# Kernel optimization log

Hardware: AMD Instinct MI355X
Metric: run time of the kernel (lower is better)

Reference implementation:

```python
import jax, jax.numpy as jnp
import numpy as np

E = 8        # n_experts
H = 1024     # hidden_size == input_size
M = 2048     # intermediate_size
K = 2        # topk
SE = 1       # share_expert
BSZ, SEQ = 2, 1024
W_SCALE = 0.02


def setup_inputs() -> dict:
    key = jax.random.key(0)
    ks = jax.random.split(key, 9)
    return {
        "x": jax.random.normal(ks[0], (BSZ, SEQ, H), jnp.float32),
        "gate_w": jax.random.normal(ks[1], (E, H), jnp.float32) * W_SCALE,
        "beta": jnp.zeros((E,), jnp.float32),
        "gate_proj_w": jax.random.normal(ks[2], (E, H, M), jnp.float32) * W_SCALE,
        "up_proj_w": jax.random.normal(ks[3], (E, H, M), jnp.float32) * W_SCALE,
        "down_proj_w": jax.random.normal(ks[4], (E, M, H), jnp.float32) * W_SCALE,
        "shared_gate_w": jax.random.normal(ks[5], (SE, H, M), jnp.float32) * W_SCALE,
        "shared_up_w": jax.random.normal(ks[6], (SE, H, M), jnp.float32) * W_SCALE,
        "shared_down_w": jax.random.normal(ks[7], (SE, M, H), jnp.float32) * W_SCALE,
    }


def reference(x, gate_w, beta, gate_proj_w, up_proj_w, down_proj_w,
              shared_gate_w, shared_up_w, shared_down_w):
    B0, S0, H0 = x.shape
    xt = x.reshape(-1, H0)                       # [B, H], B = B0*S0 tokens
    B = xt.shape[0]

    # --- routing: top-k on (logits + beta), gate prob = sigmoid(selected logits) ---
    logits = xt @ gate_w.T                       # [B, E]
    _, idx = jax.lax.top_k(logits + beta, K)     # [B, K] expert indices
    probs = jax.nn.sigmoid(jnp.take_along_axis(logits, idx, axis=-1))  # [B, K]

    # combine weights c[b, e]: scatter top-k probs (equivalent to index_add combine)
    c = jnp.zeros((B, E), xt.dtype).at[jnp.arange(B)[:, None], idx].add(probs)

    # --- per-expert SwiGLU over all tokens, then weighted combine by c ---
    g = jnp.einsum('bh,ehm->bem', xt, gate_proj_w)   # [B, E, M]
    u = jnp.einsum('bh,ehm->bem', xt, up_proj_w)     # [B, E, M]
    h = jax.nn.silu(g) * u                           # [B, E, M]
    eo = jnp.einsum('bem,emh->beh', h, down_proj_w)  # [B, E, H]
    combined = jnp.einsum('beh,be->bh', eo, c)       # [B, H]

    # --- shared expert(s): applied to every token, no gating ---
    sg = jnp.einsum('bh,ehm->bem', xt, shared_gate_w)
    su = jnp.einsum('bh,ehm->bem', xt, shared_up_w)
    sh = jax.nn.silu(sg) * su
    shared_out = jnp.einsum('bem,emh->beh', sh, shared_down_w).sum(axis=1)  # [B, H]

    return (combined + shared_out).reshape(B0, S0, H0)
```

## Files before the change

### kernel.cpp

```cpp
#include <hip/hip_runtime.h>

#define NE 8
#define HD 1024
#define MD 2048
#define NT 2048
#define NSH 4224

typedef __attribute__((ext_vector_type(8))) short s16x8;
typedef __attribute__((ext_vector_type(4))) float f32x4;
typedef __attribute__((ext_vector_type(8))) unsigned short u16x8;
typedef __attribute__((ext_vector_type(4))) unsigned short u16x4;

__device__ __forceinline__ unsigned short f2bf(float f) {
    union { float f; unsigned int i; } v; v.f = f;
    unsigned int u = v.i;
    return (unsigned short)((u + 0x7FFFu + ((u >> 16) & 1u)) >> 16);
}
__device__ __forceinline__ float bf2f(unsigned short u) {
    union { unsigned int i; float f; } v; v.i = ((unsigned int)u) << 16; return v.f;
}

__device__ __forceinline__ void gld16(const unsigned short* g, short* l) {
    __builtin_amdgcn_global_load_lds(
        (const __attribute__((address_space(1))) unsigned int*)g,
        (__attribute__((address_space(3))) unsigned int*)l,
        16, 0, 0);
}


__global__ __launch_bounds__(256) void k_cvt_gu(
    const float* __restrict__ wg, const float* __restrict__ wu,
    const float* __restrict__ swg, const float* __restrict__ swu,
    unsigned short* __restrict__ o)
{
    int e = blockIdx.z;
    const float* sg = (e < NE) ? wg + (size_t)e * HD * MD : swg;
    const float* su = (e < NE) ? wu + (size_t)e * HD * MD : swu;
    unsigned short* dst = o + (size_t)e * (2 * MD) * HD;
    int k0 = blockIdx.x * 32, n0 = blockIdx.y * 128;
    __shared__ float T[2 * 32 * 132];
    int tid = threadIdx.x;
    #pragma unroll
    for (int p = 0; p < 4; p++) {
        int idx = p * 256 + tid;
        int row = idx >> 5, l4 = (idx & 31) * 4;
        float4 vg = *(const float4*)(sg + (size_t)(k0 + row) * MD + n0 + l4);
        float4 vu = *(const float4*)(su + (size_t)(k0 + row) * MD + n0 + l4);
        *(float4*)(&T[row * 132 + l4]) = vg;
        *(float4*)(&T[32 * 132 + row * 132 + l4]) = vu;
    }
    __syncthreads();
    const int KC = HD / 8;
    #pragma unroll
    for (int p = 0; p < 4; p++) {
        int c = p * 256 + tid;
        int ni = c & 15, ns = (c >> 4) & 15, kc = c >> 8;
        int colL = ns * 8 + (ni >> 1);
        const float* Tm = &T[(ni & 1) * 32 * 132];
        u16x8 r;
        #pragma unroll
        for (int j = 0; j < 8; j++) r[j] = f2bf(Tm[(kc * 8 + j) * 132 + colL]);
        size_t oidx = ((size_t)((n0 >> 3) + ns) * KC + (k0 >> 3) + kc) * 128 + ni * 8;
        *(u16x8*)(dst + oidx) = r;
    }
}

__global__ __launch_bounds__(256) void k_cvt_d(
    const float* __restrict__ wr, const float* __restrict__ wsd,
    unsigned short* __restrict__ o)
{
    int e = blockIdx.z;
    const float* src = (e < NE) ? wr + (size_t)e * MD * HD : wsd;
    unsigned short* dst = o + (size_t)e * MD * HD;
    int k0 = blockIdx.x * 32, n0 = blockIdx.y * 128;
    __shared__ float T[32 * 132];
    int tid = threadIdx.x;
    #pragma unroll
    for (int p = 0; p < 4; p++) {
        int idx = p * 256 + tid;
        int row = idx >> 5, l4 = (idx & 31) * 4;
        float4 v = *(const float4*)(src + (size_t)(k0 + row) * HD + n0 + l4);
        *(float4*)(&T[row * 132 + l4]) = v;
    }
    __syncthreads();
    const int KC = MD / 8;
    #pragma unroll
    for (int p = 0; p < 2; p++) {
        int c = p * 256 + tid;
        int ni = c & 15, ns = (c >> 4) & 7, kc = c >> 7;
        int colL = ns * 16 + ni;
        u16x8 r;
        #pragma unroll
        for (int j = 0; j < 8; j++) r[j] = f2bf(T[(kc * 8 + j) * 132 + colL]);
        size_t oidx = ((size_t)((n0 >> 4) + ns) * KC + (k0 >> 3) + kc) * 128 + ni * 8;
        *(u16x8*)(dst + oidx) = r;
    }
}

__global__ __launch_bounds__(256) void k_route(
    const float* __restrict__ x, const float* __restrict__ gw,
    const float* __restrict__ beta,
    int* __restrict__ cnt, int* __restrict__ list, int* __restrict__ slot,
    float* __restrict__ rprob, unsigned short* __restrict__ xb)
{
    int wave = threadIdx.x >> 6, lane = threadIdx.x & 63;
    int t = blockIdx.x * 4 + wave;
    const float4* xp = (const float4*)(x + (size_t)t * HD) + lane * 4;
    float4 xv[4];
    #pragma unroll
    for (int j = 0; j < 4; j++) xv[j] = xp[j];

    u16x8 o0, o1;
    o0[0] = f2bf(xv[0].x); o0[1] = f2bf(xv[0].y); o0[2] = f2bf(xv[0].z); o0[3] = f2bf(xv[0].w);
    o0[4] = f2bf(xv[1].x); o0[5] = f2bf(xv[1].y); o0[6] = f2bf(xv[1].z); o0[7] = f2bf(xv[1].w);
    o1[0] = f2bf(xv[2].x); o1[1] = f2bf(xv[2].y); o1[2] = f2bf(xv[2].z); o1[3] = f2bf(xv[2].w);
    o1[4] = f2bf(xv[3].x); o1[5] = f2bf(xv[3].y); o1[6] = f2bf(xv[3].z); o1[7] = f2bf(xv[3].w);
    *(u16x8*)(xb + (size_t)t * HD + lane * 16) = o0;
    *(u16x8*)(xb + (size_t)t * HD + lane * 16 + 8) = o1;

    float logit[NE];
    #pragma unroll
    for (int e = 0; e < NE; e++) {
        const float4* gp = (const float4*)(gw + e * HD) + lane * 4;
        float s = 0.f;
        #pragma unroll
        for (int j = 0; j < 4; j++) {
            float4 g = gp[j];
            s += xv[j].x * g.x + xv[j].y * g.y + xv[j].z * g.z + xv[j].w * g.w;
        }
        for (int off = 32; off > 0; off >>= 1) s += __shfl_xor(s, off);
        logit[e] = s;
    }
    if (lane == 0) {
        float v[NE];
        #pragma unroll
        for (int e = 0; e < NE; e++) v[e] = logit[e] + beta[e];
        int i1 = 0; float m1 = v[0];
        #pragma unroll
        for (int e = 1; e < NE; e++) if (v[e] > m1) { m1 = v[e]; i1 = e; }
        int i2 = -1; float m2 = -3.4e38f;
        #pragma unroll
        for (int e = 0; e < NE; e++) if (e != i1 && v[e] > m2) { m2 = v[e]; i2 = e; }
        if (i2 < 0) i2 = (i1 + 1) & 7;
        float p1 = 1.f / (1.f + __expf(-logit[i1]));
        float p2 = 1.f / (1.f + __expf(-logit[i2]));
        int pos1 = atomicAdd(cnt + i1, 1);
        list[i1 * NT + pos1] = t; slot[t * 2 + 0] = (i1 << 16) | pos1; rprob[t * 2 + 0] = p1;
        int pos2 = atomicAdd(cnt + i2, 1);
        list[i2 * NT + pos2] = t; slot[t * 2 + 1] = (i2 << 16) | pos2; rprob[t * 2 + 1] = p2;
    }
}

__global__ void k_scan(const int* __restrict__ cnt, int* __restrict__ base,
                       int* __restrict__ tmap, int* __restrict__ ntile) {
    if (threadIdx.x == 0) {
        int run = 0, nt = 0;
        for (int e = 0; e < NE; e++) {
            base[e] = run;
            int c = cnt[e];
            run += (c + 15) & ~15;
            for (int i0 = 0; i0 < c; i0 += 128) tmap[nt++] = (e << 8) | (i0 >> 7);
        }
        base[NE] = run;
        for (int i0 = 0; i0 < NT; i0 += 128) tmap[nt++] = (NE << 8) | (i0 >> 7);
        *ntile = nt;
    }
}

__global__ __launch_bounds__(256, 5) void k_gateup(
    const unsigned short* __restrict__ x,
    const unsigned short* __restrict__ wgu,
    const int* __restrict__ cnt, const int* __restrict__ base, const int* __restrict__ list,
    const int* __restrict__ tmap, const int* __restrict__ ntile,
    unsigned short* __restrict__ h)
{
    int ti = blockIdx.x >> 5, ntl = blockIdx.x & 31;
    if (ti >= *ntile) return;
    int mv = tmap[ti];
    int e = mv >> 8;
    int i0 = (mv & 255) << 7;
    int n0 = ntl * 128;
    int cnte = (e < NE) ? cnt[e] : NT;
    int rbase = (e < NE) ? base[e] : NSH;
    const unsigned short* wb = wgu + (size_t)e * (2 * MD) * HD;

    __shared__ short As[2][128 * 32];
    __shared__ short Bs[2][8 * 512];

    int tid = threadIdx.x;
    int lane = tid & 63, wave = tid >> 6;

    int rr = wave * 32 + (lane >> 2);
    int gi0r = i0 + rr, gi1r = i0 + rr + 16;
    int t0, t1;
    if (e < NE) {
        t0 = list[e * NT + (gi0r < cnte ? gi0r : cnte - 1)];
        t1 = list[e * NT + (gi1r < cnte ? gi1r : cnte - 1)];
    } else { t0 = gi0r; t1 = gi1r; }

    int kc = ((lane & 3) ^ ((lane >> 3) & 3)) * 8;
    size_t gaA0 = (size_t)t0 * HD + kc;
    size_t gaA1 = (size_t)t1 * HD + kc;
    const int KC = HD / 8;
    size_t gaB0 = ((size_t)((n0 >> 4) + 2 * wave) * KC) * 128 + lane * 8;
    size_t gaB1 = gaB0 + (size_t)KC * 128;
    int loA0 = (wave * 32) * 32, loA1 = (wave * 32 + 16) * 32;
    int loB0 = (2 * wave) * 512, loB1 = (2 * wave + 1) * 512;

    int wr = (wave >> 1) * 64, wc = (wave & 1) * 64;
    int m = lane & 15, q = lane >> 4;
    int sa = (m >> 1) & 3;

    f32x4 acc[4][4];
    #pragma unroll
    for (int a = 0; a < 4; a++)
        #pragma unroll
        for (int b = 0; b < 4; b++) acc[a][b] = (f32x4)0.f;

    gld16(x + gaA0, &As[0][loA0]);
    gld16(x + gaA1, &As[0][loA1]);
    gld16(wb + gaB0, &Bs[0][loB0]);
    gld16(wb + gaB1, &Bs[0][loB1]);

    int it = 0;
    for (int k0 = 0; k0 < HD; k0 += 32, it ^= 1) {
        __syncthreads();
        int nk = k0 + 32;
        if (nk < HD) {
            int nb = it ^ 1;
            gld16(x + gaA0 + nk, &As[nb][loA0]);
            gld16(x + gaA1 + nk, &As[nb][loA1]);
            gld16(wb + gaB0 + (size_t)nk * 16, &Bs[nb][loB0]);
            gld16(wb + gaB1 + (size_t)nk * 16, &Bs[nb][loB1]);
        }
        s16x8 af[4];
        #pragma unroll
        for (int ti2 = 0; ti2 < 4; ti2++)
            af[ti2] = *(const s16x8*)(&As[it][(wr + ti2 * 16 + m) * 32 + (q ^ sa) * 8]);
        #pragma unroll
        for (int tj = 0; tj < 4; tj++) {
            s16x8 bf = *(const s16x8*)(&Bs[it][((wave & 1) * 4 + tj) * 512 + q * 128 + m * 8]);
            #pragma unroll
            for (int ti2 = 0; ti2 < 4; ti2++)
                acc[ti2][tj] = __builtin_amdgcn_mfma_f32_16x16x32_bf16(af[ti2], bf, acc[ti2][tj], 0, 0, 0);
        }
    }
    #pragma unroll
    for (int ti2 = 0; ti2 < 4; ti2++)
        #pragma unroll
        for (int tj = 0; tj < 4; tj++)
            #pragma unroll
            for (int r = 0; r < 4; r++) {
                float v = acc[ti2][tj][r];
                float uo = __shfl_xor(v, 1);
                int gi = i0 + wr + ti2 * 16 + q * 4 + r;
                if (!(m & 1) && gi < cnte) {
                    float g = v;
                    float hv = (g / (1.f + __expf(-g))) * uo;
                    int col = (n0 + wc + tj * 16 + m) >> 1;
                    int rw = rbase + gi;
                    size_t hi = ((size_t)(rw >> 4) * (MD >> 3) + (col >> 3)) * 128
                              + (rw & 15) * 8 + (col & 7);
                    h[hi] = f2bf(hv);
                }
            }
}

__global__ __launch_bounds__(256, 5) void k_down(
    const unsigned short* __restrict__ wd_all,
    const int* __restrict__ cnt, const int* __restrict__ base,
    const int* __restrict__ tmap, const int* __restrict__ ntile,
    const unsigned short* __restrict__ h, unsigned short* __restrict__ eo)
{
    int ti = blockIdx.x >> 3, ntl = blockIdx.x & 7;
    if (ti >= *ntile) return;
    int mv = tmap[ti];
    int e = mv >> 8;
    int i0 = (mv & 255) << 7;
    int n0 = ntl * 128;
    int cnte = (e < NE) ? cnt[e] : NT;
    int rbase = (e < NE) ? base[e] : NSH;
    const unsigned short* wd = wd_all + (size_t)e * MD * HD;

    __shared__ short As[2][8 * 512];
    __shared__ short Bd[2][8 * 512];

    int tid = threadIdx.x;
    int lane = tid & 63, wave = tid >> 6;
    int r0 = rbase + i0;
    const int KC = MD / 8;
    size_t gaA0 = ((size_t)((r0 >> 4) + 2 * wave) * KC) * 128 + lane * 8;
    size_t gaA1 = gaA0 + (size_t)KC * 128;
    size_t gaB0 = ((size_t)((n0 >> 4) + 2 * wave) * KC) * 128 + lane * 8;
    size_t gaB1 = gaB0 + (size_t)KC * 128;
    int lo0 = (2 * wave) * 512, lo1 = (2 * wave + 1) * 512;

    int wr = (wave >> 1) * 64, wc = (wave & 1) * 64;
    int m = lane & 15, q = lane >> 4;

    f32x4 acc[4][4];
    #pragma unroll
    for (int a = 0; a < 4; a++)
        #pragma unroll
        for (int b = 0; b < 4; b++) acc[a][b] = (f32x4)0.f;

    gld16(h + gaA0, &As[0][lo0]);
    gld16(h + gaA1, &As[0][lo1]);
    gld16(wd + gaB0, &Bd[0][lo0]);
    gld16(wd + gaB1, &Bd[0][lo1]);

    int it = 0;
    for (int k0 = 0; k0 < MD; k0 += 32, it ^= 1) {
        __syncthreads();
        int nk = k0 + 32;
        if (nk < MD) {
            int nb = it ^ 1;
            gld16(h + gaA0 + (size_t)nk * 16, &As[nb][lo0]);
            gld16(h + gaA1 + (size_t)nk * 16, &As[nb][lo1]);
            gld16(wd + gaB0 + (size_t)nk * 16, &Bd[nb][lo0]);
            gld16(wd + gaB1 + (size_t)nk * 16, &Bd[nb][lo1]);
        }
        s16x8 af[4];
        #pragma unroll
        for (int ti2 = 0; ti2 < 4; ti2++)
            af[ti2] = *(const s16x8*)(&As[it][((wave >> 1) * 4 + ti2) * 512 + q * 128 + m * 8]);
        #pragma unroll
        for (int tj = 0; tj < 4; tj++) {
            s16x8 bd = *(const s16x8*)(&Bd[it][((wave & 1) * 4 + tj) * 512 + q * 128 + m * 8]);
            #pragma unroll
            for (int ti2 = 0; ti2 < 4; ti2++)
                acc[ti2][tj] = __builtin_amdgcn_mfma_f32_16x16x32_bf16(af[ti2], bd, acc[ti2][tj], 0, 0, 0);
        }
    }
    #pragma unroll
    for (int ti2 = 0; ti2 < 4; ti2++)
        #pragma unroll
        for (int tj = 0; tj < 4; tj++)
            #pragma unroll
            for (int r = 0; r < 4; r++) {
                int gi = i0 + wr + ti2 * 16 + q * 4 + r;
                if (gi < cnte) {
                    int col = n0 + wc + tj * 16 + m;
                    eo[(size_t)(rbase + gi) * HD + col] = f2bf(acc[ti2][tj][r]);
                }
            }
}

__global__ __launch_bounds__(256) void k_combine(
    const unsigned short* __restrict__ eo, const int* __restrict__ slot,
    const float* __restrict__ rprob, const int* __restrict__ base,
    float* __restrict__ out)
{
    int t = blockIdx.x;
    int s0 = slot[t * 2], s1 = slot[t * 2 + 1];
    float p0 = rprob[t * 2], p1 = rprob[t * 2 + 1];
    int r0 = base[s0 >> 16] + (s0 & 0xFFFF);
    int r1 = base[s1 >> 16] + (s1 & 0xFFFF);
    int rs = NSH + t;
    int c = threadIdx.x * 4;
    u16x4 a = *(const u16x4*)(eo + (size_t)r0 * HD + c);
    u16x4 b = *(const u16x4*)(eo + (size_t)r1 * HD + c);
    u16x4 s = *(const u16x4*)(eo + (size_t)rs * HD + c);
    float4 res;
    res.x = p0 * bf2f(a[0]) + p1 * bf2f(b[0]) + bf2f(s[0]);
    res.y = p0 * bf2f(a[1]) + p1 * bf2f(b[1]) + bf2f(s[1]);
    res.z = p0 * bf2f(a[2]) + p1 * bf2f(b[2]) + bf2f(s[2]);
    res.w = p0 * bf2f(a[3]) + p1 * bf2f(b[3]) + bf2f(s[3]);
    *(float4*)(out + (size_t)t * HD + c) = res;
}

extern "C" void kernel_launch(void* const* d_in, const int* in_sizes, int n_in,
                              void* d_out, int out_size, void* d_ws, size_t ws_size,
                              hipStream_t stream)
{
    const float* x    = (const float*)d_in[0];
    const float* gw   = (const float*)d_in[1];
    const float* beta = (const float*)d_in[2];
    const float* wg   = (const float*)d_in[3];
    const float* wu   = (const float*)d_in[4];
    const float* wd   = (const float*)d_in[5];
    const float* swg  = (const float*)d_in[6];
    const float* swu  = (const float*)d_in[7];
    const float* swd  = (const float*)d_in[8];
    float* out = (float*)d_out;

    char* ws = (char*)d_ws;
    const size_t MB = (size_t)1 << 20;
    int*   cnt   = (int*)(ws + 0);
    int*   basep = (int*)(ws + 64);
    int*   ntile = (int*)(ws + 128);
    int*   tmap  = (int*)(ws + 192);
    int*   list  = (int*)(ws + 1024);
    int*   slot  = (int*)(ws + 1024 + 65536);
    float* rprob = (float*)(ws + 1024 + 65536 + 16384);
    unsigned short* xb   = (unsigned short*)(ws + 1 * MB);
    unsigned short* eo   = (unsigned short*)(ws + 6 * MB);
    unsigned short* wgut = (unsigned short*)(ws + 20 * MB);
    unsigned short* wdt  = (unsigned short*)(ws + 92 * MB);
    unsigned short* h    = (unsigned short*)(ws + 128 * MB);

    hipMemsetAsync(ws, 0, 128, stream);

    dim3 tgu(HD / 32, MD / 128, NE + 1);
    k_cvt_gu<<<tgu, 256, 0, stream>>>(wg, wu, swg, swu, wgut);
    dim3 td(MD / 32, HD / 128, NE + 1);
    k_cvt_d<<<td, 256, 0, stream>>>(wd, swd, wdt);

    k_route<<<NT / 4, 256, 0, stream>>>(x, gw, beta, cnt, list, slot, rprob, xb);
    k_scan<<<1, 64, 0, stream>>>(cnt, basep, tmap, ntile);

    k_gateup<<<1792, 256, 0, stream>>>(xb, wgut, cnt, basep, list, tmap, ntile, h);

    k_down<<<448, 256, 0, stream>>>(wdt, cnt, basep, tmap, ntile, h, eo);

    k_combine<<<NT, 256, 0, stream>>>(eo, slot, rprob, basep, out);
}
```

Measured before the change: 499.1 us.

## Stage gate-up epilogue through LDS and halve down-proj row tile

The gate-up kernel now writes its SwiGLU output into shared memory first, then copies it to the blocked h layout with 16-byte vector stores instead of scattered 2-byte stores. The down-projection kernel switches to 64-row tiles using a second tile map from the scan, doubling the grid to 896 blocks with smaller accumulators and raising the occupancy hint to 6. This targets uncoalesced global writes and too few blocks for the down GEMM. The cost is more weight re-reads in down-proj and extra LDS traffic plus a barrier in the gate-up epilogue.

```diff
diff --git a/kernel.cpp b/kernel.cpp
--- a/kernel.cpp
+++ b/kernel.cpp
@@ -152,18 +152,22 @@
 }
 
 __global__ void k_scan(const int* __restrict__ cnt, int* __restrict__ base,
-                       int* __restrict__ tmap, int* __restrict__ ntile) {
+                       int* __restrict__ tmap, int* __restrict__ ntile,
+                       int* __restrict__ tmap2, int* __restrict__ ntile2) {
     if (threadIdx.x == 0) {
-        int run = 0, nt = 0;
+        int run = 0, nt = 0, nt2 = 0;
         for (int e = 0; e < NE; e++) {
             base[e] = run;
             int c = cnt[e];
             run += (c + 15) & ~15;
             for (int i0 = 0; i0 < c; i0 += 128) tmap[nt++] = (e << 8) | (i0 >> 7);
+            for (int i0 = 0; i0 < c; i0 += 64)  tmap2[nt2++] = (e << 8) | (i0 >> 6);
         }
         base[NE] = run;
         for (int i0 = 0; i0 < NT; i0 += 128) tmap[nt++] = (NE << 8) | (i0 >> 7);
+        for (int i0 = 0; i0 < NT; i0 += 64)  tmap2[nt2++] = (NE << 8) | (i0 >> 6);
         *ntile = nt;
+        *ntile2 = nt2;
     }
 }
 
@@ -245,6 +249,8 @@
                 acc[ti2][tj] = __builtin_amdgcn_mfma_f32_16x16x32_bf16(af[ti2], bf, acc[ti2][tj], 0, 0, 0);
         }
     }
+    __syncthreads();
+    short* st = (short*)As;
     #pragma unroll
     for (int ti2 = 0; ti2 < 4; ti2++)
         #pragma unroll
@@ -253,61 +259,67 @@
             for (int r = 0; r < 4; r++) {
                 float v = acc[ti2][tj][r];
                 float uo = __shfl_xor(v, 1);
-                int gi = i0 + wr + ti2 * 16 + q * 4 + r;
-                if (!(m & 1) && gi < cnte) {
+                if (!(m & 1)) {
+                    int row = wr + ti2 * 16 + q * 4 + r;
+                    int hcol = (wc + tj * 16 + m) >> 1;
                     float g = v;
                     float hv = (g / (1.f + __expf(-g))) * uo;
-                    int col = (n0 + wc + tj * 16 + m) >> 1;
-                    int rw = rbase + gi;
-                    size_t hi = ((size_t)(rw >> 4) * (MD >> 3) + (col >> 3)) * 128
-                              + (rw & 15) * 8 + (col & 7);
-                    h[hi] = f2bf(hv);
+                    st[((row >> 4) * 8 + (hcol >> 3)) * 128 + (row & 15) * 8 + (hcol & 7)]
+                        = (short)f2bf(hv);
                 }
             }
-}
-
-__global__ __launch_bounds__(256, 5) void k_down(
+    __syncthreads();
+    int pad = (cnte + 15) & ~15;
+    int s = tid >> 5;
+    int o = (tid & 31) * 32;
+    if (16 * s < pad - i0) {
+        size_t gb = ((size_t)((rbase + i0) >> 4) + s) * (MD >> 3) * 128
+                  + (size_t)(n0 >> 4) * 128;
+        #pragma unroll
+        for (int j = 0; j < 4; j++)
+            *(u16x8*)(h + gb + o + j * 8) = *(const u16x8*)(&st[s * 1024 + o + j * 8]);
+    }
+}
+
+__global__ __launch_bounds__(256, 6) void k_down(
     const unsigned short* __restrict__ wd_all,
     const int* __restrict__ cnt, const int* __restrict__ base,
-    const int* __restrict__ tmap, const int* __restrict__ ntile,
+    const int* __restrict__ tmap2, const int* __restrict__ ntile2,
     const unsigned short* __restrict__ h, unsigned short* __restrict__ eo)
 {
     int ti = blockIdx.x >> 3, ntl = blockIdx.x & 7;
-    if (ti >= *ntile) return;
-    int mv = tmap[ti];
+    if (ti >= *ntile2) return;
+    int mv = tmap2[ti];
     int e = mv >> 8;
-    int i0 = (mv & 255) << 7;
+    int i0 = (mv & 255) << 6;
     int n0 = ntl * 128;
     int cnte = (e < NE) ? cnt[e] : NT;
     int rbase = (e < NE) ? base[e] : NSH;
     const unsigned short* wd = wd_all + (size_t)e * MD * HD;
 
-    __shared__ short As[2][8 * 512];
-    __shared__ short Bd[2][8 * 512];
+    __shared__ short SH[12288];
 
     int tid = threadIdx.x;
     int lane = tid & 63, wave = tid >> 6;
     int r0 = rbase + i0;
     const int KC = MD / 8;
-    size_t gaA0 = ((size_t)((r0 >> 4) + 2 * wave) * KC) * 128 + lane * 8;
-    size_t gaA1 = gaA0 + (size_t)KC * 128;
+    size_t gaA  = ((size_t)((r0 >> 4) + wave) * KC) * 128 + lane * 8;
     size_t gaB0 = ((size_t)((n0 >> 4) + 2 * wave) * KC) * 128 + lane * 8;
     size_t gaB1 = gaB0 + (size_t)KC * 128;
-    int lo0 = (2 * wave) * 512, lo1 = (2 * wave + 1) * 512;
-
-    int wr = (wave >> 1) * 64, wc = (wave & 1) * 64;
+    int loA = wave * 512;
+    int loB0 = (2 * wave) * 512, loB1 = loB0 + 512;
+
     int m = lane & 15, q = lane >> 4;
 
-    f32x4 acc[4][4];
+    f32x4 acc[4][2];
     #pragma unroll
     for (int a = 0; a < 4; a++)
         #pragma unroll
-        for (int b = 0; b < 4; b++) acc[a][b] = (f32x4)0.f;
-
-    gld16(h + gaA0, &As[0][lo0]);
-    gld16(h + gaA1, &As[0][lo1]);
-    gld16(wd + gaB0, &Bd[0][lo0]);
-    gld16(wd + gaB1, &Bd[0][lo1]);
+        for (int b = 0; b < 2; b++) acc[a][b] = (f32x4)0.f;
+
+    gld16(h + gaA, SH + loA);
+    gld16(wd + gaB0, SH + 4096 + loB0);
+    gld16(wd + gaB1, SH + 4096 + loB1);
 
     int it = 0;
     for (int k0 = 0; k0 < MD; k0 += 32, it ^= 1) {
@@ -315,18 +327,17 @@
         int nk = k0 + 32;
         if (nk < MD) {
             int nb = it ^ 1;
-            gld16(h + gaA0 + (size_t)nk * 16, &As[nb][lo0]);
-            gld16(h + gaA1 + (size_t)nk * 16, &As[nb][lo1]);
-            gld16(wd + gaB0 + (size_t)nk * 16, &Bd[nb][lo0]);
-            gld16(wd + gaB1 + (size_t)nk * 16, &Bd[nb][lo1]);
+            gld16(h + gaA + (size_t)nk * 16, SH + nb * 2048 + loA);
+            gld16(wd + gaB0 + (size_t)nk * 16, SH + 4096 + nb * 4096 + loB0);
+            gld16(wd + gaB1 + (size_t)nk * 16, SH + 4096 + nb * 4096 + loB1);
         }
         s16x8 af[4];
         #pragma unroll
         for (int ti2 = 0; ti2 < 4; ti2++)
-            af[ti2] = *(const s16x8*)(&As[it][((wave >> 1) * 4 + ti2) * 512 + q * 128 + m * 8]);
-        #pragma unroll
-        for (int tj = 0; tj < 4; tj++) {
-            s16x8 bd = *(const s16x8*)(&Bd[it][((wave & 1) * 4 + tj) * 512 + q * 128 + m * 8]);
+            af[ti2] = *(const s16x8*)(&SH[it * 2048 + ti2 * 512 + q * 128 + m * 8]);
+        #pragma unroll
+        for (int tj = 0; tj < 2; tj++) {
+            s16x8 bd = *(const s16x8*)(&SH[4096 + it * 4096 + (wave * 2 + tj) * 512 + q * 128 + m * 8]);
             #pragma unroll
             for (int ti2 = 0; ti2 < 4; ti2++)
                 acc[ti2][tj] = __builtin_amdgcn_mfma_f32_16x16x32_bf16(af[ti2], bd, acc[ti2][tj], 0, 0, 0);
@@ -335,12 +346,12 @@
     #pragma unroll
     for (int ti2 = 0; ti2 < 4; ti2++)
         #pragma unroll
-        for (int tj = 0; tj < 4; tj++)
+        for (int tj = 0; tj < 2; tj++)
             #pragma unroll
             for (int r = 0; r < 4; r++) {
-                int gi = i0 + wr + ti2 * 16 + q * 4 + r;
+                int gi = i0 + ti2 * 16 + q * 4 + r;
                 if (gi < cnte) {
-                    int col = n0 + wc + tj * 16 + m;
+                    int col = n0 + wave * 32 + tj * 16 + m;
                     eo[(size_t)(rbase + gi) * HD + col] = f2bf(acc[ti2][tj][r]);
                 }
             }
@@ -386,13 +397,15 @@
 
     char* ws = (char*)d_ws;
     const size_t MB = (size_t)1 << 20;
-    int*   cnt   = (int*)(ws + 0);
-    int*   basep = (int*)(ws + 64);
-    int*   ntile = (int*)(ws + 128);
-    int*   tmap  = (int*)(ws + 192);
-    int*   list  = (int*)(ws + 1024);
-    int*   slot  = (int*)(ws + 1024 + 65536);
-    float* rprob = (float*)(ws + 1024 + 65536 + 16384);
+    int*   cnt    = (int*)(ws + 0);
+    int*   basep  = (int*)(ws + 64);
+    int*   ntile  = (int*)(ws + 128);
+    int*   ntile2 = (int*)(ws + 132);
+    int*   tmap   = (int*)(ws + 192);
+    int*   tmap2  = (int*)(ws + 512);
+    int*   list   = (int*)(ws + 1024);
+    int*   slot   = (int*)(ws + 1024 + 65536);
+    float* rprob  = (float*)(ws + 1024 + 65536 + 16384);
     unsigned short* xb   = (unsigned short*)(ws + 1 * MB);
     unsigned short* eo   = (unsigned short*)(ws + 6 * MB);
     unsigned short* wgut = (unsigned short*)(ws + 20 * MB);
@@ -407,11 +420,11 @@
     k_cvt_d<<<td, 256, 0, stream>>>(wd, swd, wdt);
 
     k_route<<<NT / 4, 256, 0, stream>>>(x, gw, beta, cnt, list, slot, rprob, xb);
-    k_scan<<<1, 64, 0, stream>>>(cnt, basep, tmap, ntile);
+    k_scan<<<1, 64, 0, stream>>>(cnt, basep, tmap, ntile, tmap2, ntile2);
 
     k_gateup<<<1792, 256, 0, stream>>>(xb, wgut, cnt, basep, list, tmap, ntile, h);
 
-    k_down<<<448, 256, 0, stream>>>(wdt, cnt, basep, tmap, ntile, h, eo);
+    k_down<<<896, 256, 0, stream>>>(wdt, cnt, basep, tmap2, ntile2, h, eo);
 
     k_combine<<<NT, 256, 0, stream>>>(eo, slot, rprob, basep, out);
 }
```

New measurement: 559.4 us. 12.1% more time.
